# Kernel tuning notes

Hardware: AMD Instinct MI355X
Metric: run time of the kernel (lower is better)

## Reference

```python
import jax, jax.numpy as jnp
import numpy as np

B, CIN, COUT, H, W = 8, 128, 128, 64, 64

# kernel-grid base offsets (dy, dx), row-major k = kh*3 + kw, matching torch base_offset-1
BASE = jnp.array([[-1, -1], [-1, 0], [-1, 1],
                  [0, -1], [0, 0], [0, 1],
                  [1, -1], [1, 0], [1, 1]], dtype=jnp.float32)  # [9,2]
CORNER = jnp.array([1, 0, 1, 0, 0, 0, 1, 0, 1], dtype=jnp.float32)  # mask1 per kernel tap
EDGE = jnp.array([0, 1, 0, 1, 0, 1, 0, 1, 0], dtype=jnp.float32)    # mask2 per kernel tap


def conv3x3(x, w, b=None):
    out = jax.lax.conv_general_dilated(
        x, w, window_strides=(1, 1), padding=((1, 1), (1, 1)),
        dimension_numbers=('NCHW', 'OIHW', 'NCHW'))
    if b is not None:
        out = out + b[None, :, None, None]
    return out


def bilinear_sample(x, py, px):
    Bv, C, Hin, Win = x.shape
    y0 = jnp.floor(py)
    x0 = jnp.floor(px)
    wy = py - y0
    wx = px - x0
    y0i = y0.astype(jnp.int32)
    x0i = x0.astype(jnp.int32)
    xf = x.reshape(Bv, C, Hin * Win)

    def corner(yi, xi):
        valid = ((yi >= 0) & (yi < Hin) & (xi >= 0) & (xi < Win)).astype(x.dtype)
        idx = jnp.clip(yi, 0, Hin - 1) * Win + jnp.clip(xi, 0, Win - 1)  # [B,K,Ho,Wo]
        g = jax.vmap(lambda xb, ib: xb[:, ib])(xf, idx)  # [B,C,K,Ho,Wo]
        return g * valid[:, None]

    v00 = corner(y0i, x0i)
    v01 = corner(y0i, x0i + 1)
    v10 = corner(y0i + 1, x0i)
    v11 = corner(y0i + 1, x0i + 1)
    wy = wy[:, None]
    wx = wx[:, None]
    return (v00 * (1 - wy) * (1 - wx) + v01 * (1 - wy) * wx
            + v10 * wy * (1 - wx) + v11 * wy * wx)


def setup_inputs() -> dict:
    key = jax.random.key(0)
    k1, k2, k3 = jax.random.split(key, 3)
    x = jax.random.normal(k1, (B, CIN, H, W), dtype=jnp.float32)
    # small offset-conv weights keep predicted offsets in a realistic sub-pixel range
    w_off = jax.random.normal(k2, (5, CIN, 3, 3), dtype=jnp.float32) * 0.02
    b_off = jnp.zeros((5,), dtype=jnp.float32)
    w = jax.random.normal(k3, (COUT, CIN, 3, 3), dtype=jnp.float32) * (1.0 / np.sqrt(CIN * 9))
    b = jnp.zeros((COUT,), dtype=jnp.float32)
    return {"x": x, "w_off": w_off, "b_off": b_off, "w": w, "b": b}


def reference(x, w_off, b_off, w, b):
    off = conv3x3(x, w_off, b_off)          # [B,5,H,W]
    scale1 = jax.nn.relu(off[:, 2:3]) + 1.0  # corner scale [B,1,H,W]
    scale2 = jax.nn.relu(off[:, 3:4]) + 1.0  # edge scale   [B,1,H,W]
    shift = off[:, :2]                       # equivariant shift vector [B,2,H,W]

    # per-tap scale; center tap gets 0 but its base offset is (0,0) anyway
    scale_k = CORNER[None, :, None, None] * scale1 + EDGE[None, :, None, None] * scale2  # [B,9,H,W]
    # deform offset = scaled_base - base + shift = base*(scale-1) + shift
    delta = BASE[None, :, :, None, None] * (scale_k - 1.0)[:, :, None] + shift[:, None]  # [B,9,2,H,W]

    hs = jnp.arange(H, dtype=x.dtype)
    ws = jnp.arange(W, dtype=x.dtype)
    # sampling positions: p0 + base_k + offset_k (stride=1, pad=1)
    py = hs[None, None, :, None] + BASE[None, :, 0, None, None] + delta[:, :, 0]  # [B,9,H,W]
    px = ws[None, None, None, :] + BASE[None, :, 1, None, None] + delta[:, :, 1]

    sampled = bilinear_sample(x, py, px)  # [B,CIN,9,H,W]
    out = jnp.einsum('bckhw,ock->bohw', sampled, w.reshape(COUT, CIN, 9))
    return out + b[None, :, None, None]
```

## Files before the change

kernel.cpp:

```cpp
#include <hip/hip_runtime.h>

#define Wd 64
#define Hd 64
#define HWp 4096
#define CIN_ 128
#define COUT_ 128

typedef _Float16 f16;
typedef _Float16 h2    __attribute__((ext_vector_type(2)));
typedef _Float16 f16x8 __attribute__((ext_vector_type(8)));
typedef float f32x4    __attribute__((ext_vector_type(4)));

__device__ inline ushort f2h(float f) {
    f16 h = (f16)f;
    return __builtin_bit_cast(ushort, h);
}
__device__ inline h2 gb(const int4& g, int d) {
    return __builtin_bit_cast(h2, (&g.x)[d]);
}
__device__ inline h2 dup(float f) {
    f16 h = (f16)f;
    h2 r; r[0] = h; r[1] = h;
    return r;
}
struct H8 { h2 r[4]; };

__global__ __launch_bounds__(256) void prep_offsets_kernel(
    const float* __restrict__ x, const float* __restrict__ w,
    const float* __restrict__ w_off, const float* __restrict__ b_off,
    ushort* __restrict__ xt, ushort* __restrict__ w_t2,
    float4* __restrict__ der)
{
    __shared__ char smem[34816];
    int blk = blockIdx.x;
    int t = threadIdx.x;

    if (blk < 256) {
        ushort* tile = (ushort*)smem;
        int b = blk >> 5, yx0 = (blk & 31) << 7;
        const float* xb = x + (size_t)b * CIN_ * HWp + yx0;
        int lanelo = t & 31, grp = t >> 5;
        #pragma unroll
        for (int i = 0; i < 4; i++) {
            int cbase = i * 32 + grp * 4;
            float4 v0 = *(const float4*)(xb + (size_t)(cbase + 0) * HWp + lanelo * 4);
            float4 v1 = *(const float4*)(xb + (size_t)(cbase + 1) * HWp + lanelo * 4);
            float4 v2 = *(const float4*)(xb + (size_t)(cbase + 2) * HWp + lanelo * 4);
            float4 v3 = *(const float4*)(xb + (size_t)(cbase + 3) * HWp + lanelo * 4);
            ushort4 u;
            u.x = f2h(v0.x); u.y = f2h(v1.x); u.z = f2h(v2.x); u.w = f2h(v3.x);
            *(ushort4*)&tile[(lanelo * 4 + 0) * 136 + cbase] = u;
            u.x = f2h(v0.y); u.y = f2h(v1.y); u.z = f2h(v2.y); u.w = f2h(v3.y);
            *(ushort4*)&tile[(lanelo * 4 + 1) * 136 + cbase] = u;
            u.x = f2h(v0.z); u.y = f2h(v1.z); u.z = f2h(v2.z); u.w = f2h(v3.z);
            *(ushort4*)&tile[(lanelo * 4 + 2) * 136 + cbase] = u;
            u.x = f2h(v0.w); u.y = f2h(v1.w); u.z = f2h(v2.w); u.w = f2h(v3.w);
            *(ushort4*)&tile[(lanelo * 4 + 3) * 136 + cbase] = u;
        }
        __syncthreads();
        ushort* dst = xt + ((size_t)b * HWp + yx0) * CIN_;
        int c8 = (t & 15) * 8, yxg = t >> 4;
        #pragma unroll
        for (int i = 0; i < 8; i++) {
            int yxl = i * 16 + yxg;
            int4 v = *(int4*)&tile[yxl * 136 + c8];
            *(int4*)(dst + (size_t)yxl * CIN_ + c8) = v;
        }
    } else if (blk < 832) {
        int i = (blk - 256) * 256 + t;
        int j    = i & 7;
        int lane = (i >> 3) & 63;
        int ii   = (i >> 9) & 3;
        int wm   = (i >> 11) & 1;
        int s    = i >> 12;
        int o = wm * 64 + ii * 16 + (lane & 15);
        int c = (s & 3) * 32 + (lane >> 4) * 8 + j;
        int k = s >> 2;
        w_t2[i] = f2h(w[o * 1152 + c * 9 + k]);
    } else {
        float* wl   = (float*)smem;
        float* part = (float*)(smem + 18432);
        int blk2 = blk - 832;
        int b = blk2 >> 6;
        int h = blk2 & 63;

        for (int i = t; i < 4608; i += 256) {
            int j = i / 1152;
            int r = i - j * 1152;
            wl[r * 4 + j] = w_off[i];
        }
        __syncthreads();

        int pi = t & 63, cc = t >> 6;
        const float* xb = x + (size_t)(b * CIN_ + cc * 32) * HWp;

        int idx9[9];
        float msk9[9];
        #pragma unroll
        for (int dy = 0; dy < 3; dy++) {
            int hy = h + dy - 1;
            int hyc = min(max(hy, 0), Hd - 1);
            bool vr = (hy >= 0) && (hy < Hd);
            #pragma unroll
            for (int dx = 0; dx < 3; dx++) {
                int wx = pi + dx - 1;
                int wxc = min(max(wx, 0), Wd - 1);
                bool v = vr && (wx >= 0) && (wx < Wd);
                idx9[dy * 3 + dx] = hyc * Wd + wxc;
                msk9[dy * 3 + dx] = v ? 1.0f : 0.0f;
            }
        }

        float o0 = 0.f, o1 = 0.f, o2 = 0.f, o3 = 0.f;
        #pragma unroll 4
        for (int c = 0; c < 32; c++) {
            const float* xp = xb + c * HWp;
            const float* wc = &wl[(cc * 32 + c) * 36];
            float xv[9];
            #pragma unroll
            for (int tp = 0; tp < 9; tp++) xv[tp] = xp[idx9[tp]] * msk9[tp];
            #pragma unroll
            for (int tp = 0; tp < 9; tp++) {
                float4 wj = *(const float4*)&wc[tp * 4];
                o0 += xv[tp] * wj.x; o1 += xv[tp] * wj.y;
                o2 += xv[tp] * wj.z; o3 += xv[tp] * wj.w;
            }
        }
        part[t * 4 + 0] = o0;
        part[t * 4 + 1] = o1;
        part[t * 4 + 2] = o2;
        part[t * 4 + 3] = o3;
        __syncthreads();

        if (t < 64) {
            float s0 = b_off[0], s1 = b_off[1], s2 = b_off[2], s3 = b_off[3];
            #pragma unroll
            for (int q = 0; q < 4; q++) {
                s0 += part[(q * 64 + t) * 4 + 0];
                s1 += part[(q * 64 + t) * 4 + 1];
                s2 += part[(q * 64 + t) * 4 + 2];
                s3 += part[(q * 64 + t) * 4 + 3];
            }
            float4 d;
            d.x = s0;
            d.y = s1;
            d.z = fmaxf(s2, 0.f) + 1.f;
            d.w = fmaxf(s3, 0.f) + 1.f;
            der[(size_t)b * HWp + h * Wd + t] = d;
        }
    }
}

__global__ __launch_bounds__(256, 2) void deform_gemm_mfma(
    const ushort* __restrict__ xt, const ushort* __restrict__ w_t2,
    const float* __restrict__ bias, const float4* __restrict__ der,
    float* __restrict__ out)
{
    __shared__ ushort A_lds[2][2][4096];
    __shared__ ushort S_lds[2][2][64 * 40];
    __shared__ int4 MI[9][64];
    __shared__ int4 MW[9][64];

    int t = threadIdx.x;
    int b = blockIdx.x & 7;
    int rp = blockIdx.x >> 3;
    int p0 = rp << 6;
    const char* xtb = (const char*)(xt + (size_t)b * HWp * CIN_);

    int p  = t >> 2;
    int c8 = (t & 3) << 3;
    int c8b = c8 * 2;

    int wv = t >> 6, lane = t & 63;
    int wm = wv & 1, ns = wv >> 1;
    int lm = lane & 15, lq = lane >> 4;

    f32x4 acc[4][2] = {};

    {
        int pg = p0 + p;
        float fh = (float)(pg >> 6), fp = (float)(pg & 63);
        float4 dv = der[(size_t)b * HWp + pg];
        for (int k = (t & 3); k < 9; k += 4) {
            int ky = (k * 11) >> 5;
            int kx = k - ky * 3;
            float by = (float)(ky - 1), bx = (float)(kx - 1);
            bool corner = (ky != 1) && (kx != 1);
            bool edge = (ky != 1) ^ (kx != 1);
            float sk = corner ? dv.z : (edge ? dv.w : 0.0f);
            float py = fh + by * sk + dv.x;
            float px = fp + bx * sk + dv.y;
            float y0f = floorf(py), x0f = floorf(px);
            float wy = py - y0f, wx = px - x0f;
            int y0 = (int)y0f, x0 = (int)x0f;
            int y1 = y0 + 1, x1 = x0 + 1;
            float vy0 = (y0 >= 0 && y0 < Hd) ? 1.f : 0.f;
            float vy1 = (y1 >= 0 && y1 < Hd) ? 1.f : 0.f;
            float vx0 = (x0 >= 0 && x0 < Wd) ? 1.f : 0.f;
            float vx1 = (x1 >= 0 && x1 < Wd) ? 1.f : 0.f;
            int cy0 = min(max(y0, 0), Hd - 1), cy1 = min(max(y1, 0), Hd - 1);
            int cx0 = min(max(x0, 0), Wd - 1), cx1 = min(max(x1, 0), Wd - 1);
            int4 ii;
            ii.x = (cy0 * Wd + cx0) << 8;
            ii.y = (cy0 * Wd + cx1) << 8;
            ii.z = (cy1 * Wd + cx0) << 8;
            ii.w = (cy1 * Wd + cx1) << 8;
            MI[k][p] = ii;
            H8 hw;
            hw.r[0] = dup((1.f - wy) * (1.f - wx) * vy0 * vx0);
            hw.r[1] = dup((1.f - wy) * wx * vy0 * vx1);
            hw.r[2] = dup(wy * (1.f - wx) * vy1 * vx0);
            hw.r[3] = dup(wy * wx * vy1 * vx1);
            MW[k][p] = __builtin_bit_cast(int4, hw);
        }
    }
    __syncthreads();

    int vo0, vo1, vo2, vo3;

    auto stageA = [&](int buf, int st) {
        const ushort* src = w_t2 + (size_t)st * 8192;
        #pragma unroll
        for (int cc = 0; cc < 2; cc++) {
            #pragma unroll
            for (int hrow = 0; hrow < 2; hrow++) {
                const ushort* g = src + cc * 4096 + (wv * 2 + hrow) * 512 + lane * 8;
                ushort* l = &A_lds[buf][cc][(wv * 2 + hrow) * 512];
                __builtin_amdgcn_global_load_lds(
                    (const __attribute__((address_space(1))) unsigned int*)g,
                    (__attribute__((address_space(3))) unsigned int*)l, 16, 0, 0);
            }
        }
    };

    auto issue = [&](int st, int4 (&G)[2][4]) {
        #pragma unroll
        for (int cc = 0; cc < 2; cc++) {
            int q = (2 * st + cc) & 3;
            G[cc][0] = *(const int4*)(xtb + (vo0 + q * 64));
            G[cc][1] = *(const int4*)(xtb + (vo1 + q * 64));
            G[cc][2] = *(const int4*)(xtb + (vo2 + q * 64));
            G[cc][3] = *(const int4*)(xtb + (vo3 + q * 64));
        }
    };
    auto commitS = [&](int buf, const int4 (&G)[2][4], const H8& cw) {
        #pragma unroll
        for (int cc = 0; cc < 2; cc++) {
            H8 tmp;
            #pragma unroll
            for (int d = 0; d < 4; d++) {
                h2 r = gb(G[cc][0], d) * cw.r[0];
                r = gb(G[cc][1], d) * cw.r[1] + r;
                r = gb(G[cc][2], d) * cw.r[2] + r;
                r = gb(G[cc][3], d) * cw.r[3] + r;
                tmp.r[d] = r;
            }
            *(int4*)&S_lds[buf][cc][p * 40 + c8] = __builtin_bit_cast(int4, tmp);
        }
    };
    auto mfmaSec = [&](int cur) {
        #pragma unroll
        for (int cc = 0; cc < 2; cc++) {
            f16x8 af[4], bfr[2];
            #pragma unroll
            for (int i = 0; i < 4; i++)
                af[i] = *(const f16x8*)&A_lds[cur][cc][(wm * 4 + i) * 512 + lane * 8];
            #pragma unroll
            for (int f = 0; f < 2; f++)
                bfr[f] = *(const f16x8*)&S_lds[cur][cc][(ns * 32 + f * 16 + lm) * 40 + lq * 8];
            #pragma unroll
            for (int i = 0; i < 4; i++)
                #pragma unroll
                for (int f = 0; f < 2; f++)
                    acc[i][f] = __builtin_amdgcn_mfma_f32_16x16x32_f16(
                        af[i], bfr[f], acc[i][f], 0, 0, 0);
        }
    };

    int4 GA[2][4], GB[2][4];
    H8 cwA, cwB;
    int4 idxN;

    stageA(0, 0);
    __builtin_amdgcn_sched_barrier(0);
    {
        int4 i0 = MI[0][p];
        vo0 = i0.x + c8b; vo1 = i0.y + c8b; vo2 = i0.z + c8b; vo3 = i0.w + c8b;
    }
    issue(0, GA);
    cwA = __builtin_bit_cast(H8, MW[0][p]);
    commitS(0, GA, cwA);
    issue(1, GB);
    idxN = MI[1][p];
    asm volatile("s_waitcnt vmcnt(8) lgkmcnt(0)" ::: "memory");
    __builtin_amdgcn_s_barrier();
    __builtin_amdgcn_sched_barrier(0);

#define BODY(ST, GC, GI, CWC, CWR, DORD)                                     \
    {                                                                        \
        int cur_ = (ST) & 1, nb_ = cur_ ^ 1;                                 \
        if ((ST) + 1 < 18) stageA(nb_, (ST) + 1);                            \
        __builtin_amdgcn_sched_barrier(0);                                   \
        if ((ST) + 2 < 18) {                                                 \
            if (DORD) {                                                      \
                vo0 = idxN.x + c8b; vo1 = idxN.y + c8b;                      \
                vo2 = idxN.z + c8b; vo3 = idxN.w + c8b;                      \
            }                                                                \
            issue((ST) + 2, GI);                                             \
        }                                                                    \
        if (DORD) {                                                          \
            idxN = MI[min(((ST) >> 1) + 2, 8)][p];                           \
            CWR = __builtin_bit_cast(H8, MW[min(((ST) >> 1) + 1, 8)][p]);    \
        }                                                                    \
        __builtin_amdgcn_s_setprio(1);                                       \
        mfmaSec(cur_);                                                       \
        __builtin_amdgcn_s_setprio(0);                                       \
        if ((ST) + 1 < 18) commitS(nb_, GC, CWC);                            \
        if ((ST) + 2 < 18) {                                                 \
            asm volatile("s_waitcnt vmcnt(8) lgkmcnt(0)" ::: "memory");      \
        } else {                                                             \
            asm volatile("s_waitcnt vmcnt(0) lgkmcnt(0)" ::: "memory");      \
        }                                                                    \
        __builtin_amdgcn_s_barrier();                                        \
        __builtin_amdgcn_sched_barrier(0);                                   \
    }

    for (int su = 0; su < 4; su++) {
        int st = su << 2;
        BODY(st,     GB, GA, cwA, cwB, 1);
        BODY(st + 1, GA, GB, cwB, cwB, 0);
        BODY(st + 2, GB, GA, cwB, cwA, 1);
        BODY(st + 3, GA, GB, cwA, cwA, 0);
    }
    BODY(16, GB, GA, cwA, cwB, 1);
    BODY(17, GA, GB, cwB, cwB, 0);
#undef BODY

    #pragma unroll
    for (int i = 0; i < 4; i++) {
        #pragma unroll
        for (int r = 0; r < 4; r++) {
            int o = wm * 64 + i * 16 + lq * 4 + r;
            float bv = bias[o];
            float* orow = out + (size_t)(b * COUT_ + o) * HWp + p0 + ns * 32 + lm;
            #pragma unroll
            for (int f = 0; f < 2; f++)
                __builtin_nontemporal_store(acc[i][f][r] + bv, &orow[f * 16]);
        }
    }
}

extern "C" void kernel_launch(void* const* d_in, const int* in_sizes, int n_in,
                              void* d_out, int out_size, void* d_ws, size_t ws_size,
                              hipStream_t stream) {
    const float* x     = (const float*)d_in[0];
    const float* w_off = (const float*)d_in[1];
    const float* b_off = (const float*)d_in[2];
    const float* w     = (const float*)d_in[3];
    const float* bias  = (const float*)d_in[4];
    float* out = (float*)d_out;

    char* ws = (char*)d_ws;
    ushort* xt   = (ushort*)ws;
    ushort* w_t2 = (ushort*)(ws + 8388608);
    float4* der  = (float4*)(ws + 8683520);

    prep_offsets_kernel<<<1344, 256, 0, stream>>>(x, w, w_off, b_off,
                                                  xt, w_t2, der);
    deform_gemm_mfma<<<512, 256, 0, stream>>>(xt, w_t2, bias, der, out);
}
```

Baseline: 114.6 us.

## Build bilinear B fragments in registers, drop sampled-tile LDS staging

Each wave now gathers and bilinearly blends its own 16 pixel columns straight into the MFMA B-operand layout, so the sampled tile no longer goes through a shared-memory round trip. Each wave computes all 128 output channels for its 16 pixels instead of sharing a 2x2 wave split. This removes the S_lds buffer and its LDS writes and reads, and raises the launch-bounds occupancy target from 2 to 3 blocks. In exchange every wave re-reads all of A from LDS per chunk, and the gather loads are now finer-grained with tighter vmcnt waits.

```diff
diff --git a/kernel.cpp b/kernel.cpp
--- a/kernel.cpp
+++ b/kernel.cpp
@@ -151,13 +151,12 @@
     }
 }
 
-__global__ __launch_bounds__(256, 2) void deform_gemm_mfma(
+__global__ __launch_bounds__(256, 3) void deform_gemm_mfma(
     const ushort* __restrict__ xt, const ushort* __restrict__ w_t2,
     const float* __restrict__ bias, const float4* __restrict__ der,
     float* __restrict__ out)
 {
     __shared__ ushort A_lds[2][2][4096];
-    __shared__ ushort S_lds[2][2][64 * 40];
     __shared__ int4 MI[9][64];
     __shared__ int4 MW[9][64];
 
@@ -167,17 +166,15 @@
     int p0 = rp << 6;
     const char* xtb = (const char*)(xt + (size_t)b * HWp * CIN_);
 
-    int p  = t >> 2;
-    int c8 = (t & 3) << 3;
-    int c8b = c8 * 2;
-
     int wv = t >> 6, lane = t & 63;
-    int wm = wv & 1, ns = wv >> 1;
     int lm = lane & 15, lq = lane >> 4;
-
-    f32x4 acc[4][2] = {};
+    int myp = wv * 16 + lm;
+    int lqb = lq * 16;
+
+    f32x4 acc[8] = {};
 
     {
+        int p = t >> 2;
         int pg = p0 + p;
         float fh = (float)(pg >> 6), fp = (float)(pg & 63);
         float4 dv = der[(size_t)b * HWp + pg];
@@ -233,119 +230,109 @@
         }
     };
 
-    auto issue = [&](int st, int4 (&G)[2][4]) {
-        #pragma unroll
-        for (int cc = 0; cc < 2; cc++) {
-            int q = (2 * st + cc) & 3;
-            G[cc][0] = *(const int4*)(xtb + (vo0 + q * 64));
-            G[cc][1] = *(const int4*)(xtb + (vo1 + q * 64));
-            G[cc][2] = *(const int4*)(xtb + (vo2 + q * 64));
-            G[cc][3] = *(const int4*)(xtb + (vo3 + q * 64));
-        }
+    auto issueG = [&](int4 (&G)[4], int qm) {
+        int off = qm * 64;
+        G[0] = *(const int4*)(xtb + (vo0 + off));
+        G[1] = *(const int4*)(xtb + (vo1 + off));
+        G[2] = *(const int4*)(xtb + (vo2 + off));
+        G[3] = *(const int4*)(xtb + (vo3 + off));
     };
-    auto commitS = [&](int buf, const int4 (&G)[2][4], const H8& cw) {
-        #pragma unroll
-        for (int cc = 0; cc < 2; cc++) {
-            H8 tmp;
-            #pragma unroll
-            for (int d = 0; d < 4; d++) {
-                h2 r = gb(G[cc][0], d) * cw.r[0];
-                r = gb(G[cc][1], d) * cw.r[1] + r;
-                r = gb(G[cc][2], d) * cw.r[2] + r;
-                r = gb(G[cc][3], d) * cw.r[3] + r;
-                tmp.r[d] = r;
-            }
-            *(int4*)&S_lds[buf][cc][p * 40 + c8] = __builtin_bit_cast(int4, tmp);
-        }
+
+    auto mfmaChunk = [&](int cur, int cc, const int4 (&G)[4], const H8& cw) {
+        H8 tmp;
+        #pragma unroll
+        for (int d = 0; d < 4; d++) {
+            h2 r = gb(G[0], d) * cw.r[0];
+            r = gb(G[1], d) * cw.r[1] + r;
+            r = gb(G[2], d) * cw.r[2] + r;
+            r = gb(G[3], d) * cw.r[3] + r;
+            tmp.r[d] = r;
+        }
+        f16x8 bf = __builtin_bit_cast(f16x8, tmp);
+        __builtin_amdgcn_s_setprio(1);
+        #pragma unroll
+        for (int i = 0; i < 8; i++) {
+            f16x8 af = *(const f16x8*)&A_lds[cur][cc][i * 512 + lane * 8];
+            acc[i] = __builtin_amdgcn_mfma_f32_16x16x32_f16(af, bf, acc[i], 0, 0, 0);
+        }
+        __builtin_amdgcn_s_setprio(0);
     };
-    auto mfmaSec = [&](int cur) {
-        #pragma unroll
-        for (int cc = 0; cc < 2; cc++) {
-            f16x8 af[4], bfr[2];
-            #pragma unroll
-            for (int i = 0; i < 4; i++)
-                af[i] = *(const f16x8*)&A_lds[cur][cc][(wm * 4 + i) * 512 + lane * 8];
-            #pragma unroll
-            for (int f = 0; f < 2; f++)
-                bfr[f] = *(const f16x8*)&S_lds[cur][cc][(ns * 32 + f * 16 + lm) * 40 + lq * 8];
-            #pragma unroll
-            for (int i = 0; i < 4; i++)
-                #pragma unroll
-                for (int f = 0; f < 2; f++)
-                    acc[i][f] = __builtin_amdgcn_mfma_f32_16x16x32_f16(
-                        af[i], bfr[f], acc[i][f], 0, 0, 0);
-        }
-    };
-
-    int4 GA[2][4], GB[2][4];
+
+    int4 GA[4], GB[4];
     H8 cwA, cwB;
     int4 idxN;
 
+    {
+        int4 mi0 = MI[0][myp];
+        vo0 = mi0.x + lqb; vo1 = mi0.y + lqb; vo2 = mi0.z + lqb; vo3 = mi0.w + lqb;
+        cwA = __builtin_bit_cast(H8, MW[0][myp]);
+        idxN = MI[1][myp];
+    }
     stageA(0, 0);
     __builtin_amdgcn_sched_barrier(0);
-    {
-        int4 i0 = MI[0][p];
-        vo0 = i0.x + c8b; vo1 = i0.y + c8b; vo2 = i0.z + c8b; vo3 = i0.w + c8b;
-    }
-    issue(0, GA);
-    cwA = __builtin_bit_cast(H8, MW[0][p]);
-    commitS(0, GA, cwA);
-    issue(1, GB);
-    idxN = MI[1][p];
-    asm volatile("s_waitcnt vmcnt(8) lgkmcnt(0)" ::: "memory");
+    issueG(GA, 0);
+    asm volatile("s_waitcnt vmcnt(4)" ::: "memory");
     __builtin_amdgcn_s_barrier();
     __builtin_amdgcn_sched_barrier(0);
 
-#define BODY(ST, GC, GI, CWC, CWR, DORD)                                     \
+#define BODY(ST, CWC, CWN, DORD)                                             \
     {                                                                        \
         int cur_ = (ST) & 1, nb_ = cur_ ^ 1;                                 \
-        if ((ST) + 1 < 18) stageA(nb_, (ST) + 1);                            \
-        __builtin_amdgcn_sched_barrier(0);                                   \
-        if ((ST) + 2 < 18) {                                                 \
-            if (DORD) {                                                      \
-                vo0 = idxN.x + c8b; vo1 = idxN.y + c8b;                      \
-                vo2 = idxN.z + c8b; vo3 = idxN.w + c8b;                      \
-            }                                                                \
-            issue((ST) + 2, GI);                                             \
+        issueG(GB, (2 * (ST) + 1) & 3);                                      \
+        stageA(nb_, (ST) + 1);                                               \
+        __builtin_amdgcn_sched_barrier(0);                                   \
+        asm volatile("s_waitcnt vmcnt(8)" ::: "memory");                     \
+        __builtin_amdgcn_sched_barrier(0);                                   \
+        mfmaChunk(cur_, 0, GA, CWC);                                         \
+        if (DORD) {                                                          \
+            vo0 = idxN.x + lqb; vo1 = idxN.y + lqb;                          \
+            vo2 = idxN.z + lqb; vo3 = idxN.w + lqb;                          \
         }                                                                    \
+        issueG(GA, (2 * (ST) + 2) & 3);                                      \
         if (DORD) {                                                          \
-            idxN = MI[min(((ST) >> 1) + 2, 8)][p];                           \
-            CWR = __builtin_bit_cast(H8, MW[min(((ST) >> 1) + 1, 8)][p]);    \
+            idxN = MI[min(((ST) >> 1) + 2, 8)][myp];                         \
+            CWN  = __builtin_bit_cast(H8, MW[min(((ST) >> 1) + 1, 8)][myp]); \
         }                                                                    \
-        __builtin_amdgcn_s_setprio(1);                                       \
-        mfmaSec(cur_);                                                       \
-        __builtin_amdgcn_s_setprio(0);                                       \
-        if ((ST) + 1 < 18) commitS(nb_, GC, CWC);                            \
-        if ((ST) + 2 < 18) {                                                 \
-            asm volatile("s_waitcnt vmcnt(8) lgkmcnt(0)" ::: "memory");      \
-        } else {                                                             \
-            asm volatile("s_waitcnt vmcnt(0) lgkmcnt(0)" ::: "memory");      \
-        }                                                                    \
+        __builtin_amdgcn_sched_barrier(0);                                   \
+        asm volatile("s_waitcnt vmcnt(8)" ::: "memory");                     \
+        __builtin_amdgcn_sched_barrier(0);                                   \
+        mfmaChunk(cur_, 1, GB, CWC);                                         \
+        asm volatile("s_waitcnt vmcnt(4)" ::: "memory");                     \
         __builtin_amdgcn_s_barrier();                                        \
         __builtin_amdgcn_sched_barrier(0);                                   \
     }
 
     for (int su = 0; su < 4; su++) {
         int st = su << 2;
-        BODY(st,     GB, GA, cwA, cwB, 1);
-        BODY(st + 1, GA, GB, cwB, cwB, 0);
-        BODY(st + 2, GB, GA, cwB, cwA, 1);
-        BODY(st + 3, GA, GB, cwA, cwA, 0);
-    }
-    BODY(16, GB, GA, cwA, cwB, 1);
-    BODY(17, GA, GB, cwB, cwB, 0);
+        BODY(st,     cwA, cwB, 0);
+        BODY(st + 1, cwA, cwB, 1);
+        BODY(st + 2, cwB, cwA, 0);
+        BODY(st + 3, cwB, cwA, 1);
+    }
+    BODY(16, cwA, cwB, 0);
 #undef BODY
 
+    {
+        issueG(GB, 3);
+        __builtin_amdgcn_sched_barrier(0);
+        asm volatile("s_waitcnt vmcnt(4)" ::: "memory");
+        __builtin_amdgcn_sched_barrier(0);
+        mfmaChunk(1, 0, GA, cwA);
+        asm volatile("s_waitcnt vmcnt(0)" ::: "memory");
+        __builtin_amdgcn_sched_barrier(0);
+        mfmaChunk(1, 1, GB, cwA);
+    }
+
+    int pgo = p0 + wv * 16 + lm;
     #pragma unroll
-    for (int i = 0; i < 4; i++) {
+    for (int I = 0; I < 8; I++) {
+        int ob = (I >> 2) * 64 + (I & 3) * 16 + lq * 4;
         #pragma unroll
         for (int r = 0; r < 4; r++) {
-            int o = wm * 64 + i * 16 + lq * 4 + r;
+            int o = ob + r;
             float bv = bias[o];
-            float* orow = out + (size_t)(b * COUT_ + o) * HWp + p0 + ns * 32 + lm;
-            #pragma unroll
-            for (int f = 0; f < 2; f++)
-                __builtin_nontemporal_store(acc[i][f][r] + bv, &orow[f * 16]);
+            __builtin_nontemporal_store(acc[I][r] + bv,
+                out + (size_t)(b * COUT_ + o) * HWp + pgo);
         }
     }
 }
```

New measurement: 131.5 us. 1.15x slower.
